# Kernel tuning notes

Measured on AMD Instinct MI355X. Metric: run time of the kernel, lower is better.

Reference implementation:

```python
import jax, jax.numpy as jnp
import numpy as np

N_USERS = 100000
M_ITEMS = 50000
D = 64
NNZ = 4_000_000
B = 4096
LAYERS = 3


def setup_inputs() -> dict:
    key = jax.random.key(0)
    ks = jax.random.split(key, 7)
    N = N_USERS + M_ITEMS
    return {
        "users": jax.random.randint(ks[0], (B,), 0, N_USERS, dtype=jnp.int64 if jax.config.jax_enable_x64 else jnp.int32),
        "items": jax.random.randint(ks[1], (B,), 0, M_ITEMS, dtype=jnp.int64 if jax.config.jax_enable_x64 else jnp.int32),
        "user_emb": jax.random.normal(ks[2], (N_USERS, D), dtype=jnp.float32) * 0.1,
        "item_emb": jax.random.normal(ks[3], (M_ITEMS, D), dtype=jnp.float32) * 0.1,
        "adj_rows": jax.random.randint(ks[4], (NNZ,), 0, N, dtype=jnp.int32),
        "adj_cols": jax.random.randint(ks[5], (NNZ,), 0, N, dtype=jnp.int32),
        "adj_vals": jax.random.uniform(ks[6], (NNZ,), dtype=jnp.float32),
    }


def reference(users, items, user_emb, item_emb, adj_rows, adj_cols, adj_vals):
    n_users = user_emb.shape[0]
    N = n_users + item_emb.shape[0]

    # computer(): multi-layer sparse propagation, mean over layer outputs
    all_emb = jnp.concatenate([user_emb, item_emb], axis=0)  # [N, D]
    acc = all_emb
    emb = all_emb
    for _ in range(LAYERS):
        # SpMM as gather + segment-sum: (A @ emb)[r] = sum_{e: row(e)=r} val(e) * emb[col(e)]
        messages = adj_vals[:, None] * emb[adj_cols]          # [NNZ, D]
        emb = jax.ops.segment_sum(messages, adj_rows, num_segments=N)
        acc = acc + emb
    light_out = acc / (LAYERS + 1)                            # mean over stacked layers

    all_users = light_out[:n_users]
    all_items = light_out[n_users:]

    # forward(users, items)
    u = all_users[users]                                      # [B, D]
    i = all_items[items]                                      # [B, D]
    gamma = jnp.sum(u * i, axis=1)                            # [B]
    return gamma
```

## Files before the change

### kernel.cpp

```cpp
#include <hip/hip_runtime.h>

#define N_USERS 100000
#define M_ITEMS 50000
#define N_TOTAL (N_USERS + M_ITEMS)
#define D 64
#define NNZ 4000000
#define BATCH 4096

#define RPB 128
#define BSHIFT 7
#define NBUCKETS ((N_TOTAL + RPB - 1) / RPB)
#define BCAP 7680

#define TILE 8192
#define SCAT_BLOCKS ((NNZ + TILE - 1) / TILE)
#define SCAT_THREADS 512
#define EPT (TILE / SCAT_THREADS)
#define CPB 3

#define LS_THREADS 512
#define LS_EPT 16

__device__ __forceinline__ unsigned pack_bf16(float a, float b) {
    unsigned ua = __float_as_uint(a);
    unsigned ub = __float_as_uint(b);
    ua = (ua + 0x7FFFu + ((ua >> 16) & 1u)) >> 16;
    ub = (ub + 0x7FFFu + ((ub >> 16) & 1u)) & 0xFFFF0000u;
    return ua | ub;
}
__device__ __forceinline__ float bf16_lo(unsigned p) { return __uint_as_float(p << 16); }
__device__ __forceinline__ float bf16_hi(unsigned p) { return __uint_as_float(p & 0xFFFF0000u); }


__global__ void init_emb_kernel(const float4* __restrict__ ue,
                                const float4* __restrict__ ie,
                                uint2* __restrict__ emb) {
    size_t i = (size_t)blockIdx.x * blockDim.x + threadIdx.x;
    const size_t nu4  = (size_t)N_USERS * D / 4;
    const size_t tot4 = (size_t)N_TOTAL * D / 4;
    if (i >= tot4) return;
    float4 f = (i < nu4) ? ue[i] : ie[i - nu4];
    emb[i] = make_uint2(pack_bf16(f.x, f.y), pack_bf16(f.z, f.w));
}

__global__ void init_acc_kernel(const int* __restrict__ users,
                                const int* __restrict__ items,
                                const float* __restrict__ ue,
                                const float* __restrict__ ie,
                                float* __restrict__ u_acc,
                                float* __restrict__ i_acc) {
    int gid = blockIdx.x * blockDim.x + threadIdx.x;
    int d = gid & (D - 1);
    int b = gid >> 6;
    if (b < BATCH) {
        u_acc[(size_t)b * D + d] = ue[(size_t)users[b] * D + d];
    } else if (b < 2 * BATCH) {
        int bb = b - BATCH;
        i_acc[(size_t)bb * D + d] = ie[(size_t)items[bb] * D + d];
    }
}


__global__ void bucket_hist_kernel(const int* __restrict__ rows,
                                   int* __restrict__ bucketcnt) {
    __shared__ int h[NBUCKETS];
    for (int i = threadIdx.x; i < NBUCKETS; i += blockDim.x) h[i] = 0;
    __syncthreads();
    int stride = gridDim.x * blockDim.x;
    for (int e = blockIdx.x * blockDim.x + threadIdx.x; e < NNZ; e += stride)
        atomicAdd(&h[rows[e] >> BSHIFT], 1);
    __syncthreads();
    for (int i = threadIdx.x; i < NBUCKETS; i += blockDim.x)
        if (h[i]) atomicAdd(&bucketcnt[i], h[i]);
}

__global__ void bucket_scan_kernel(const int* __restrict__ cnt,
                                   int* __restrict__ bucketoff,
                                   int* __restrict__ cursor) {
    __shared__ int sc[1024];
    int t = threadIdx.x;
    int i0 = t * 2, i1 = t * 2 + 1;
    int a = (i0 < NBUCKETS) ? cnt[i0] : 0;
    int b = (i1 < NBUCKETS) ? cnt[i1] : 0;
    sc[t] = a + b;
    __syncthreads();
    for (int o = 1; o < 1024; o <<= 1) {
        int v = (t >= o) ? sc[t - o] : 0;
        __syncthreads();
        sc[t] += v;
        __syncthreads();
    }
    int excl = (t == 0) ? 0 : sc[t - 1];
    if (i0 < NBUCKETS) { bucketoff[i0] = excl;     cursor[i0] = excl; }
    if (i1 < NBUCKETS) { bucketoff[i1] = excl + a; cursor[i1] = excl + a; }
    if (t == 0) bucketoff[NBUCKETS] = NNZ;
}

__global__ __launch_bounds__(SCAT_THREADS)
void bucket_scatter_kernel(const int* __restrict__ rows,
                           const int* __restrict__ cols,
                           const float* __restrict__ vals,
                           int* __restrict__ cursor,
                           int2* __restrict__ bucketed) {
    __shared__ int hist[NBUCKETS];
    __shared__ int loff[NBUCKETS + 1];
    __shared__ int partial[SCAT_THREADS];
    __shared__ int2 buf[TILE];
    int t = threadIdx.x;
    size_t start = (size_t)blockIdx.x * TILE;
    int n = (int)(((size_t)NNZ - start < TILE) ? ((size_t)NNZ - start) : TILE);

    for (int i = t; i < NBUCKETS; i += SCAT_THREADS) hist[i] = 0;
    __syncthreads();
    int rowv[EPT];
    int rank[EPT];
#pragma unroll
    for (int k = 0; k < EPT; ++k) {
        int i = t + k * SCAT_THREADS;
        if (i < n) {
            int r = rows[start + i];
            rowv[k] = r;
            rank[k] = atomicAdd(&hist[r >> BSHIFT], 1);
        }
    }
    __syncthreads();
    {
        int base = t * CPB;
        int s = 0;
#pragma unroll
        for (int j = 0; j < CPB; ++j) {
            int idx = base + j;
            if (idx < NBUCKETS) s += hist[idx];
        }
        partial[t] = s;
        __syncthreads();
        for (int o = 1; o < SCAT_THREADS; o <<= 1) {
            int v = (t >= o) ? partial[t - o] : 0;
            __syncthreads();
            partial[t] += v;
            __syncthreads();
        }
        int excl = (t == 0) ? 0 : partial[t - 1];
#pragma unroll
        for (int j = 0; j < CPB; ++j) {
            int idx = base + j;
            if (idx < NBUCKETS) { loff[idx] = excl; excl += hist[idx]; }
        }
        if (t == 0) loff[NBUCKETS] = n;
    }
    __syncthreads();
    for (int i = t; i < NBUCKETS; i += SCAT_THREADS) {
        int c = loff[i + 1] - loff[i];
        hist[i] = c ? atomicAdd(&cursor[i], c) : 0;
    }
    __syncthreads();
#pragma unroll
    for (int k = 0; k < EPT; ++k) {
        int i = t + k * SCAT_THREADS;
        if (i < n) {
            int r = rowv[k];
            buf[loff[r >> BSHIFT] + rank[k]] =
                make_int2(((r & (RPB - 1)) << 18) | cols[start + i],
                          __float_as_int(vals[start + i]));
        }
    }
    __syncthreads();
    for (int b = t; b < NBUCKETS; b += SCAT_THREADS) {
        int lo = loff[b], hi = loff[b + 1];
        int gb = hist[b];
        for (int i = lo; i < hi; ++i)
            bucketed[gb + (i - lo)] = buf[i];
    }
}

__global__ __launch_bounds__(LS_THREADS)
void local_sort_kernel(const int* __restrict__ bucketoff,
                       const int2* __restrict__ bucketed,
                       int* __restrict__ row_start,
                       int2* __restrict__ edges) {
    __shared__ int hist[RPB];
    __shared__ int sc[RPB];
    __shared__ int2 buf[BCAP];
    int b = blockIdx.x;
    int t = threadIdx.x;
    int s = bucketoff[b], e = bucketoff[b + 1], n = e - s;

    if (t < RPB) hist[t] = 0;
    __syncthreads();
    int rank[LS_EPT];
    int rl[LS_EPT];
#pragma unroll
    for (int k = 0; k < LS_EPT; ++k) {
        int i = t + k * LS_THREADS;
        if (i < n) {
            int2 ev = bucketed[s + i];
            rl[k] = (int)((unsigned)ev.x >> 18);
            rank[k] = atomicAdd(&hist[rl[k]], 1);
        }
    }
    __syncthreads();
    if (t < RPB) sc[t] = hist[t];
    __syncthreads();
    for (int o = 1; o < RPB; o <<= 1) {
        int v = (t < RPB && t >= o) ? sc[t - o] : 0;
        __syncthreads();
        if (t < RPB) sc[t] += v;
        __syncthreads();
    }
    if (t < RPB) {
        int excl = (t == 0) ? 0 : sc[t - 1];
        int gr = b * RPB + t;
        if (gr < N_TOTAL) row_start[gr] = s + excl;
    }
    if (b == 0 && t == 0) row_start[N_TOTAL] = NNZ;
    __syncthreads();
#pragma unroll
    for (int k = 0; k < LS_EPT; ++k) {
        int i = t + k * LS_THREADS;
        if (i < n) {
            int2 ev = bucketed[s + i];
            int r = rl[k];
            int excl = (r == 0) ? 0 : sc[r - 1];
            int p = excl + rank[k];
            int2 outv = make_int2((ev.x & 0x3FFFF) << 7, ev.y);
            if (p < BCAP) buf[p] = outv;
            else          edges[s + p] = outv;
        }
    }
    __syncthreads();
    int m = (n < BCAP) ? n : BCAP;
    for (int i = t; i < m; i += LS_THREADS) edges[s + i] = buf[i];
}

__global__ void spmm_csr_kernel(const int* __restrict__ row_start,
                                const int2* __restrict__ edges,
                                const char* __restrict__ emb_in,
                                uint2* __restrict__ emb_out) {
    int wave = (blockIdx.x * blockDim.x + threadIdx.x) >> 6;
    int lane = threadIdx.x & 63;
    if (wave >= N_TOTAL) return;
    int quad = lane >> 4;
    int ui   = lane & 15;
    int s = row_start[wave];
    int e = row_start[wave + 1];
    float a0 = 0.f, a1 = 0.f, a2 = 0.f, a3 = 0.f;
    for (int base = s; base < e; base += 64) {
        int n = e - base; if (n > 64) n = 64;
        int c = 0; float v = 0.0f;
        if (base + lane < e) {
            int2 ev = edges[base + lane];
            c = ev.x; v = __int_as_float(ev.y);
        }
        int tmax = (n + 3) >> 2;
        for (int t = 0; t < tmax; ++t) {
            int j = 4 * t + quad;
            int   cj = __shfl(c, j, 64);
            float vj = __shfl(v, j, 64);
            float m  = (j < n) ? vj : 0.0f;
            uint2 p = *(const uint2*)(emb_in + cj + 8 * ui);
            a0 += m * bf16_lo(p.x);
            a1 += m * bf16_hi(p.x);
            a2 += m * bf16_lo(p.y);
            a3 += m * bf16_hi(p.y);
        }
    }
    a0 += __shfl_xor(a0, 16, 64); a1 += __shfl_xor(a1, 16, 64);
    a2 += __shfl_xor(a2, 16, 64); a3 += __shfl_xor(a3, 16, 64);
    a0 += __shfl_xor(a0, 32, 64); a1 += __shfl_xor(a1, 32, 64);
    a2 += __shfl_xor(a2, 32, 64); a3 += __shfl_xor(a3, 32, 64);
    if (quad == 0)
        emb_out[(size_t)wave * 16 + ui] = make_uint2(pack_bf16(a0, a1),
                                                     pack_bf16(a2, a3));
}

__global__ void layer3_kernel(const int* __restrict__ users,
                              const int* __restrict__ items,
                              const int* __restrict__ row_start,
                              const int2* __restrict__ edges,
                              const char* __restrict__ emb_in,
                              float* __restrict__ u_acc,
                              float* __restrict__ i_acc) {
    int wave = (blockIdx.x * blockDim.x + threadIdx.x) >> 6;
    int lane = threadIdx.x & 63;
    if (wave >= 2 * BATCH) return;
    int quad = lane >> 4;
    int ui   = lane & 15;
    int row;
    float* dst;
    if (wave < BATCH) {
        row = users[wave];
        dst = &u_acc[(size_t)wave * D];
    } else {
        int bb = wave - BATCH;
        row = N_USERS + items[bb];
        dst = &i_acc[(size_t)bb * D];
    }
    int s = row_start[row];
    int e = row_start[row + 1];
    float a0 = 0.f, a1 = 0.f, a2 = 0.f, a3 = 0.f;
    for (int base = s; base < e; base += 64) {
        int n = e - base; if (n > 64) n = 64;
        int c = 0; float v = 0.0f;
        if (base + lane < e) {
            int2 ev = edges[base + lane];
            c = ev.x; v = __int_as_float(ev.y);
        }
        int tmax = (n + 3) >> 2;
        for (int t = 0; t < tmax; ++t) {
            int j = 4 * t + quad;
            int   cj = __shfl(c, j, 64);
            float vj = __shfl(v, j, 64);
            float m  = (j < n) ? vj : 0.0f;
            uint2 p = *(const uint2*)(emb_in + cj + 8 * ui);
            a0 += m * bf16_lo(p.x);
            a1 += m * bf16_hi(p.x);
            a2 += m * bf16_lo(p.y);
            a3 += m * bf16_hi(p.y);
        }
    }
    a0 += __shfl_xor(a0, 16, 64); a1 += __shfl_xor(a1, 16, 64);
    a2 += __shfl_xor(a2, 16, 64); a3 += __shfl_xor(a3, 16, 64);
    a0 += __shfl_xor(a0, 32, 64); a1 += __shfl_xor(a1, 32, 64);
    a2 += __shfl_xor(a2, 32, 64); a3 += __shfl_xor(a3, 32, 64);
    if (quad == 0) {
        dst[4 * ui + 0] += a0;
        dst[4 * ui + 1] += a1;
        dst[4 * ui + 2] += a2;
        dst[4 * ui + 3] += a3;
    }
}

__global__ void gather_acc_kernel(const int* __restrict__ users,
                                  const int* __restrict__ items,
                                  const unsigned* __restrict__ emb,
                                  float* __restrict__ u_acc,
                                  float* __restrict__ i_acc) {
    int gid = blockIdx.x * blockDim.x + threadIdx.x;
    int ui = gid & 31;
    int b  = gid >> 5;
    if (b < BATCH) {
        unsigned p = emb[(size_t)users[b] * 32 + ui];
        u_acc[(size_t)b * D + 2 * ui]     += bf16_lo(p);
        u_acc[(size_t)b * D + 2 * ui + 1] += bf16_hi(p);
    } else if (b < 2 * BATCH) {
        int bb = b - BATCH;
        unsigned p = emb[((size_t)(N_USERS + items[bb])) * 32 + ui];
        i_acc[(size_t)bb * D + 2 * ui]     += bf16_lo(p);
        i_acc[(size_t)bb * D + 2 * ui + 1] += bf16_hi(p);
    }
}

__global__ void final_dot_kernel(const float* __restrict__ u_acc,
                                 const float* __restrict__ i_acc,
                                 float* __restrict__ out) {
    int gid = blockIdx.x * blockDim.x + threadIdx.x;
    int b = gid >> 6;
    int lane = gid & 63;
    if (b >= BATCH) return;
    float p = u_acc[(size_t)b * D + lane] * i_acc[(size_t)b * D + lane];
#pragma unroll
    for (int o = 32; o; o >>= 1) p += __shfl_xor(p, o, 64);
    if (lane == 0) out[b] = p * (1.0f / 16.0f);
}


extern "C" void kernel_launch(void* const* d_in, const int* in_sizes, int n_in,
                              void* d_out, int out_size, void* d_ws, size_t ws_size,
                              hipStream_t stream) {
    const int*   users = (const int*)d_in[0];
    const int*   items = (const int*)d_in[1];
    const float* ue    = (const float*)d_in[2];
    const float* ie    = (const float*)d_in[3];
    const int*   rows  = (const int*)d_in[4];
    const int*   cols  = (const int*)d_in[5];
    const float* vals  = (const float*)d_in[6];
    float*       out   = (float*)d_out;

    char* ws = (char*)d_ws;
    size_t off = 0;
    auto alloc = [&](size_t bytes) {
        void* p = ws + off;
        off += (bytes + 255) & ~(size_t)255;
        return p;
    };
    const size_t NBH = (size_t)N_TOTAL * D * sizeof(unsigned short);
    char*  embA      = (char*)alloc(NBH);
    char*  embB      = (char*)alloc(NBH);
    float* u_acc     = (float*)alloc((size_t)BATCH * D * sizeof(float));
    float* i_acc     = (float*)alloc((size_t)BATCH * D * sizeof(float));
    int*   row_start = (int*)alloc(((size_t)N_TOTAL + 1) * sizeof(int));
    int*   bucketcnt = (int*)alloc((size_t)NBUCKETS * sizeof(int));
    int*   bucketoff = (int*)alloc(((size_t)NBUCKETS + 1) * sizeof(int));
    int*   cursor    = (int*)alloc((size_t)NBUCKETS * sizeof(int));
    int2*  edges     = (int2*)alloc((size_t)NNZ * sizeof(int2));
    int2*  bucketed  = (int2*)alloc((size_t)NNZ * sizeof(int2));

    {
        size_t tot4 = (size_t)N_TOTAL * D / 4;
        init_emb_kernel<<<(unsigned)((tot4 + 255) / 256), 256, 0, stream>>>(
            (const float4*)ue, (const float4*)ie, (uint2*)embA);
        init_acc_kernel<<<(2 * BATCH * D + 255) / 256, 256, 0, stream>>>(
            users, items, ue, ie, u_acc, i_acc);
    }

    hipMemsetAsync(bucketcnt, 0, (size_t)NBUCKETS * sizeof(int), stream);
    bucket_hist_kernel<<<512, 256, 0, stream>>>(rows, bucketcnt);
    bucket_scan_kernel<<<1, 1024, 0, stream>>>(bucketcnt, bucketoff, cursor);
    bucket_scatter_kernel<<<SCAT_BLOCKS, SCAT_THREADS, 0, stream>>>(
        rows, cols, vals, cursor, bucketed);
    local_sort_kernel<<<NBUCKETS, LS_THREADS, 0, stream>>>(
        bucketoff, bucketed, row_start, edges);

    spmm_csr_kernel<<<(N_TOTAL * 64 + 255) / 256, 256, 0, stream>>>(
        row_start, edges, embA, (uint2*)embB);
    gather_acc_kernel<<<(2 * BATCH * 32 + 255) / 256, 256, 0, stream>>>(
        users, items, (const unsigned*)embB, u_acc, i_acc);

    spmm_csr_kernel<<<(N_TOTAL * 64 + 255) / 256, 256, 0, stream>>>(
        row_start, edges, embB, (uint2*)embA);
    gather_acc_kernel<<<(2 * BATCH * 32 + 255) / 256, 256, 0, stream>>>(
        users, items, (const unsigned*)embA, u_acc, i_acc);

    layer3_kernel<<<(2 * BATCH * 64 + 255) / 256, 256, 0, stream>>>(
        users, items, row_start, edges, embA, u_acc, i_acc);

    final_dot_kernel<<<(BATCH * 64 + 255) / 256, 256, 0, stream>>>(u_acc, i_acc, out);
}
```

Baseline: 409.9 us.

## Switch SpMM to fp16 packed FMA with rows padded to multiples of four

Embeddings and edge values are stored as fp16, and SpMM accumulates with packed half2 FMA instead of fp32 with bf16 unpacking. Each CSR row is padded to a multiple of four edges with zero entries, so the inner loop drops the shuffle broadcast and bounds masking and loads edges directly per quad. The bucket scatter now writes through a precomputed per-slot destination in parallel instead of a serial per-bucket copy. The risk is fp16 accumulation overflow or precision loss on rows with many neighbours, plus the extra padded edge storage.

```diff
diff --git a/kernel.cpp b/kernel.cpp
--- a/kernel.cpp
+++ b/kernel.cpp
@@ -1,4 +1,5 @@
 #include <hip/hip_runtime.h>
+#include <hip/hip_fp16.h>
 
 #define N_USERS 100000
 #define M_ITEMS 50000
@@ -11,6 +12,7 @@
 #define BSHIFT 7
 #define NBUCKETS ((N_TOTAL + RPB - 1) / RPB)
 #define BCAP 7680
+#define PADB 384
 
 #define TILE 8192
 #define SCAT_BLOCKS ((NNZ + TILE - 1) / TILE)
@@ -21,15 +23,12 @@
 #define LS_THREADS 512
 #define LS_EPT 16
 
-__device__ __forceinline__ unsigned pack_bf16(float a, float b) {
-    unsigned ua = __float_as_uint(a);
-    unsigned ub = __float_as_uint(b);
-    ua = (ua + 0x7FFFu + ((ua >> 16) & 1u)) >> 16;
-    ub = (ub + 0x7FFFu + ((ub >> 16) & 1u)) & 0xFFFF0000u;
-    return ua | ub;
-}
-__device__ __forceinline__ float bf16_lo(unsigned p) { return __uint_as_float(p << 16); }
-__device__ __forceinline__ float bf16_hi(unsigned p) { return __uint_as_float(p & 0xFFFF0000u); }
+__device__ __forceinline__ __half2 u2h2(unsigned u) {
+    union { unsigned u; __half2 h; } x; x.u = u; return x.h;
+}
+__device__ __forceinline__ unsigned h22u(__half2 h) {
+    union { unsigned u; __half2 h; } x; x.h = h; return x.u;
+}
 
 
 __global__ void init_emb_kernel(const float4* __restrict__ ue,
@@ -40,7 +39,9 @@
     const size_t tot4 = (size_t)N_TOTAL * D / 4;
     if (i >= tot4) return;
     float4 f = (i < nu4) ? ue[i] : ie[i - nu4];
-    emb[i] = make_uint2(pack_bf16(f.x, f.y), pack_bf16(f.z, f.w));
+    __half2 h01 = __float22half2_rn(make_float2(f.x, f.y));
+    __half2 h23 = __float22half2_rn(make_float2(f.z, f.w));
+    emb[i] = make_uint2(h22u(h01), h22u(h23));
 }
 
 __global__ void init_acc_kernel(const int* __restrict__ users,
@@ -106,6 +107,7 @@
     __shared__ int loff[NBUCKETS + 1];
     __shared__ int partial[SCAT_THREADS];
     __shared__ int2 buf[TILE];
+    __shared__ int dst[TILE];
     int t = threadIdx.x;
     size_t start = (size_t)blockIdx.x * TILE;
     int n = (int)(((size_t)NNZ - start < TILE) ? ((size_t)NNZ - start) : TILE);
@@ -159,18 +161,16 @@
         int i = t + k * SCAT_THREADS;
         if (i < n) {
             int r = rowv[k];
-            buf[loff[r >> BSHIFT] + rank[k]] =
-                make_int2(((r & (RPB - 1)) << 18) | cols[start + i],
-                          __float_as_int(vals[start + i]));
-        }
-    }
-    __syncthreads();
-    for (int b = t; b < NBUCKETS; b += SCAT_THREADS) {
-        int lo = loff[b], hi = loff[b + 1];
-        int gb = hist[b];
-        for (int i = lo; i < hi; ++i)
-            bucketed[gb + (i - lo)] = buf[i];
-    }
+            int bkt = r >> BSHIFT;
+            int slot = loff[bkt] + rank[k];
+            buf[slot] = make_int2(((r & (RPB - 1)) << 18) | cols[start + i],
+                                  __float_as_int(vals[start + i]));
+            dst[slot] = hist[bkt] + rank[k];
+        }
+    }
+    __syncthreads();
+    for (int i = t; i < n; i += SCAT_THREADS)
+        bucketed[dst[i]] = buf[i];
 }
 
 __global__ __launch_bounds__(LS_THREADS)
@@ -184,22 +184,27 @@
     int b = blockIdx.x;
     int t = threadIdx.x;
     int s = bucketoff[b], e = bucketoff[b + 1], n = e - s;
-
+    int cap = n + PADB;
+
+    for (int i = t; i < cap; i += LS_THREADS) buf[i] = make_int2(0, 0);
     if (t < RPB) hist[t] = 0;
     __syncthreads();
-    int rank[LS_EPT];
-    int rl[LS_EPT];
+    int rl[LS_EPT], rank[LS_EPT];
+    int2 pay[LS_EPT];
 #pragma unroll
     for (int k = 0; k < LS_EPT; ++k) {
         int i = t + k * LS_THREADS;
         if (i < n) {
             int2 ev = bucketed[s + i];
             rl[k] = (int)((unsigned)ev.x >> 18);
+            float v = __int_as_float(ev.y);
+            unsigned hv = (unsigned)__half_as_ushort(__float2half(v));
+            pay[k] = make_int2((ev.x & 0x3FFFF) << 7, (int)(hv | (hv << 16)));
             rank[k] = atomicAdd(&hist[rl[k]], 1);
         }
     }
     __syncthreads();
-    if (t < RPB) sc[t] = hist[t];
+    if (t < RPB) sc[t] = (hist[t] + 3) & ~3;
     __syncthreads();
     for (int o = 1; o < RPB; o <<= 1) {
         int v = (t < RPB && t >= o) ? sc[t - o] : 0;
@@ -207,29 +212,24 @@
         if (t < RPB) sc[t] += v;
         __syncthreads();
     }
+    int pbase = s + b * PADB;
     if (t < RPB) {
         int excl = (t == 0) ? 0 : sc[t - 1];
         int gr = b * RPB + t;
-        if (gr < N_TOTAL) row_start[gr] = s + excl;
-    }
-    if (b == 0 && t == 0) row_start[N_TOTAL] = NNZ;
+        if (gr < N_TOTAL) row_start[gr] = pbase + excl;
+    }
+    if (b == 0 && t == 0) row_start[N_TOTAL] = NNZ + NBUCKETS * PADB;
     __syncthreads();
 #pragma unroll
     for (int k = 0; k < LS_EPT; ++k) {
         int i = t + k * LS_THREADS;
         if (i < n) {
-            int2 ev = bucketed[s + i];
-            int r = rl[k];
-            int excl = (r == 0) ? 0 : sc[r - 1];
-            int p = excl + rank[k];
-            int2 outv = make_int2((ev.x & 0x3FFFF) << 7, ev.y);
-            if (p < BCAP) buf[p] = outv;
-            else          edges[s + p] = outv;
-        }
-    }
-    __syncthreads();
-    int m = (n < BCAP) ? n : BCAP;
-    for (int i = t; i < m; i += LS_THREADS) edges[s + i] = buf[i];
+            int excl = (rl[k] == 0) ? 0 : sc[rl[k] - 1];
+            buf[excl + rank[k]] = pay[k];
+        }
+    }
+    __syncthreads();
+    for (int i = t; i < cap; i += LS_THREADS) edges[pbase + i] = buf[i];
 }
 
 __global__ void spmm_csr_kernel(const int* __restrict__ row_start,
@@ -243,34 +243,23 @@
     int ui   = lane & 15;
     int s = row_start[wave];
     int e = row_start[wave + 1];
-    float a0 = 0.f, a1 = 0.f, a2 = 0.f, a3 = 0.f;
-    for (int base = s; base < e; base += 64) {
-        int n = e - base; if (n > 64) n = 64;
-        int c = 0; float v = 0.0f;
-        if (base + lane < e) {
-            int2 ev = edges[base + lane];
-            c = ev.x; v = __int_as_float(ev.y);
-        }
-        int tmax = (n + 3) >> 2;
-        for (int t = 0; t < tmax; ++t) {
-            int j = 4 * t + quad;
-            int   cj = __shfl(c, j, 64);
-            float vj = __shfl(v, j, 64);
-            float m  = (j < n) ? vj : 0.0f;
-            uint2 p = *(const uint2*)(emb_in + cj + 8 * ui);
-            a0 += m * bf16_lo(p.x);
-            a1 += m * bf16_hi(p.x);
-            a2 += m * bf16_lo(p.y);
-            a3 += m * bf16_hi(p.y);
-        }
-    }
-    a0 += __shfl_xor(a0, 16, 64); a1 += __shfl_xor(a1, 16, 64);
-    a2 += __shfl_xor(a2, 16, 64); a3 += __shfl_xor(a3, 16, 64);
-    a0 += __shfl_xor(a0, 32, 64); a1 += __shfl_xor(a1, 32, 64);
-    a2 += __shfl_xor(a2, 32, 64); a3 += __shfl_xor(a3, 32, 64);
+    int cnt = (e - s) >> 2;
+    const int2* ep = edges + s + quad;
+    int uioff = ui << 3;
+    __half2 a01 = u2h2(0u), a23 = u2h2(0u);
+    for (int t = 0; t < cnt; ++t) {
+        int2 ev = ep[4 * t];
+        uint2 p = *(const uint2*)(emb_in + ev.x + uioff);
+        __half2 m2 = u2h2((unsigned)ev.y);
+        a01 = __hfma2(m2, u2h2(p.x), a01);
+        a23 = __hfma2(m2, u2h2(p.y), a23);
+    }
+    a01 = __hadd2(a01, u2h2(__shfl_xor(h22u(a01), 16, 64)));
+    a23 = __hadd2(a23, u2h2(__shfl_xor(h22u(a23), 16, 64)));
+    a01 = __hadd2(a01, u2h2(__shfl_xor(h22u(a01), 32, 64)));
+    a23 = __hadd2(a23, u2h2(__shfl_xor(h22u(a23), 32, 64)));
     if (quad == 0)
-        emb_out[(size_t)wave * 16 + ui] = make_uint2(pack_bf16(a0, a1),
-                                                     pack_bf16(a2, a3));
+        emb_out[(size_t)wave * 16 + ui] = make_uint2(h22u(a01), h22u(a23));
 }
 
 __global__ void layer3_kernel(const int* __restrict__ users,
@@ -286,67 +275,59 @@
     int quad = lane >> 4;
     int ui   = lane & 15;
     int row;
-    float* dst;
+    float* dstp;
     if (wave < BATCH) {
         row = users[wave];
-        dst = &u_acc[(size_t)wave * D];
+        dstp = &u_acc[(size_t)wave * D];
     } else {
         int bb = wave - BATCH;
         row = N_USERS + items[bb];
-        dst = &i_acc[(size_t)bb * D];
+        dstp = &i_acc[(size_t)bb * D];
     }
     int s = row_start[row];
     int e = row_start[row + 1];
-    float a0 = 0.f, a1 = 0.f, a2 = 0.f, a3 = 0.f;
-    for (int base = s; base < e; base += 64) {
-        int n = e - base; if (n > 64) n = 64;
-        int c = 0; float v = 0.0f;
-        if (base + lane < e) {
-            int2 ev = edges[base + lane];
-            c = ev.x; v = __int_as_float(ev.y);
-        }
-        int tmax = (n + 3) >> 2;
-        for (int t = 0; t < tmax; ++t) {
-            int j = 4 * t + quad;
-            int   cj = __shfl(c, j, 64);
-            float vj = __shfl(v, j, 64);
-            float m  = (j < n) ? vj : 0.0f;
-            uint2 p = *(const uint2*)(emb_in + cj + 8 * ui);
-            a0 += m * bf16_lo(p.x);
-            a1 += m * bf16_hi(p.x);
-            a2 += m * bf16_lo(p.y);
-            a3 += m * bf16_hi(p.y);
-        }
-    }
-    a0 += __shfl_xor(a0, 16, 64); a1 += __shfl_xor(a1, 16, 64);
-    a2 += __shfl_xor(a2, 16, 64); a3 += __shfl_xor(a3, 16, 64);
-    a0 += __shfl_xor(a0, 32, 64); a1 += __shfl_xor(a1, 32, 64);
-    a2 += __shfl_xor(a2, 32, 64); a3 += __shfl_xor(a3, 32, 64);
+    int cnt = (e - s) >> 2;
+    const int2* ep = edges + s + quad;
+    int uioff = ui << 3;
+    __half2 a01 = u2h2(0u), a23 = u2h2(0u);
+    for (int t = 0; t < cnt; ++t) {
+        int2 ev = ep[4 * t];
+        uint2 p = *(const uint2*)(emb_in + ev.x + uioff);
+        __half2 m2 = u2h2((unsigned)ev.y);
+        a01 = __hfma2(m2, u2h2(p.x), a01);
+        a23 = __hfma2(m2, u2h2(p.y), a23);
+    }
+    a01 = __hadd2(a01, u2h2(__shfl_xor(h22u(a01), 16, 64)));
+    a23 = __hadd2(a23, u2h2(__shfl_xor(h22u(a23), 16, 64)));
+    a01 = __hadd2(a01, u2h2(__shfl_xor(h22u(a01), 32, 64)));
+    a23 = __hadd2(a23, u2h2(__shfl_xor(h22u(a23), 32, 64)));
     if (quad == 0) {
-        dst[4 * ui + 0] += a0;
-        dst[4 * ui + 1] += a1;
-        dst[4 * ui + 2] += a2;
-        dst[4 * ui + 3] += a3;
+        float2 f01 = __half22float2(a01);
+        float2 f23 = __half22float2(a23);
+        dstp[4 * ui + 0] += f01.x;
+        dstp[4 * ui + 1] += f01.y;
+        dstp[4 * ui + 2] += f23.x;
+        dstp[4 * ui + 3] += f23.y;
     }
 }
 
 __global__ void gather_acc_kernel(const int* __restrict__ users,
                                   const int* __restrict__ items,
-                                  const unsigned* __restrict__ emb,
+                                  const __half2* __restrict__ emb,
                                   float* __restrict__ u_acc,
                                   float* __restrict__ i_acc) {
     int gid = blockIdx.x * blockDim.x + threadIdx.x;
     int ui = gid & 31;
     int b  = gid >> 5;
     if (b < BATCH) {
-        unsigned p = emb[(size_t)users[b] * 32 + ui];
-        u_acc[(size_t)b * D + 2 * ui]     += bf16_lo(p);
-        u_acc[(size_t)b * D + 2 * ui + 1] += bf16_hi(p);
+        float2 f = __half22float2(emb[(size_t)users[b] * 32 + ui]);
+        u_acc[(size_t)b * D + 2 * ui]     += f.x;
+        u_acc[(size_t)b * D + 2 * ui + 1] += f.y;
     } else if (b < 2 * BATCH) {
         int bb = b - BATCH;
-        unsigned p = emb[((size_t)(N_USERS + items[bb])) * 32 + ui];
-        i_acc[(size_t)bb * D + 2 * ui]     += bf16_lo(p);
-        i_acc[(size_t)bb * D + 2 * ui + 1] += bf16_hi(p);
+        float2 f = __half22float2(emb[((size_t)(N_USERS + items[bb])) * 32 + ui]);
+        i_acc[(size_t)bb * D + 2 * ui]     += f.x;
+        i_acc[(size_t)bb * D + 2 * ui + 1] += f.y;
     }
 }
 
@@ -384,6 +365,7 @@
         return p;
     };
     const size_t NBH = (size_t)N_TOTAL * D * sizeof(unsigned short);
+    const size_t NEDGE = (size_t)NNZ + (size_t)NBUCKETS * PADB;
     char*  embA      = (char*)alloc(NBH);
     char*  embB      = (char*)alloc(NBH);
     float* u_acc     = (float*)alloc((size_t)BATCH * D * sizeof(float));
@@ -392,7 +374,7 @@
     int*   bucketcnt = (int*)alloc((size_t)NBUCKETS * sizeof(int));
     int*   bucketoff = (int*)alloc(((size_t)NBUCKETS + 1) * sizeof(int));
     int*   cursor    = (int*)alloc((size_t)NBUCKETS * sizeof(int));
-    int2*  edges     = (int2*)alloc((size_t)NNZ * sizeof(int2));
+    int2*  edges     = (int2*)alloc(NEDGE * sizeof(int2));
     int2*  bucketed  = (int2*)alloc((size_t)NNZ * sizeof(int2));
 
     {
@@ -414,12 +396,12 @@
     spmm_csr_kernel<<<(N_TOTAL * 64 + 255) / 256, 256, 0, stream>>>(
         row_start, edges, embA, (uint2*)embB);
     gather_acc_kernel<<<(2 * BATCH * 32 + 255) / 256, 256, 0, stream>>>(
-        users, items, (const unsigned*)embB, u_acc, i_acc);
+        users, items, (const __half2*)embB, u_acc, i_acc);
 
     spmm_csr_kernel<<<(N_TOTAL * 64 + 255) / 256, 256, 0, stream>>>(
         row_start, edges, embB, (uint2*)embA);
     gather_acc_kernel<<<(2 * BATCH * 32 + 255) / 256, 256, 0, stream>>>(
-        users, items, (const unsigned*)embA, u_acc, i_acc);
+        users, items, (const __half2*)embA, u_acc, i_acc);
 
     layer3_kernel<<<(2 * BATCH * 64 + 255) / 256, 256, 0, stream>>>(
         users, items, row_start, edges, embA, u_acc, i_acc);
```

Result: slower. 779.7 us (+90.2%).
